# Performance work log

Measured on AMD Instinct MI355X. Metric: run time of the kernel, lower is better.

Reference implementation:

```python
import jax, jax.numpy as jnp
import numpy as np

B, N, C, H = 2, 2048, 1024, 16
D = C // H  # head_dim = 64
EPS = 1e-6


def _rope_freqs(n, d):
    inv_freq = 1.0 / (10000.0 ** (np.arange(0, d // 2, dtype=np.float32) * 2.0 / d))
    ang = np.arange(n, dtype=np.float32)[:, None] * inv_freq[None, :]  # [N, D/2]
    ang = np.concatenate([ang, ang], axis=-1)  # [N, D] (chunk-in-half convention)
    cos = jnp.asarray(np.cos(ang))[None, None]  # [1,1,N,D]
    sin = jnp.asarray(np.sin(ang))[None, None]
    return cos, sin


def setup_inputs() -> dict:
    key = jax.random.key(0)
    k1, k2, k3 = jax.random.split(key, 3)
    x = jax.random.normal(k1, (B, N, C), dtype=jnp.float32)
    w_qkv = jax.random.normal(k2, (3 * C, C), dtype=jnp.float32) * (C ** -0.5)
    w_proj = jax.random.normal(k3, (C, C), dtype=jnp.float32) * (C ** -0.5)
    b_proj = jnp.zeros((C,), dtype=jnp.float32)
    freqs_cos, freqs_sin = _rope_freqs(N, D)
    return {"x": x, "w_qkv": w_qkv, "w_proj": w_proj, "b_proj": b_proj,
            "freqs_cos": freqs_cos, "freqs_sin": freqs_sin}


def _layernorm(t):
    # affine-free LayerNorm over the last (head_dim) axis
    mu = jnp.mean(t, axis=-1, keepdims=True)
    var = jnp.var(t, axis=-1, keepdims=True)
    return (t - mu) * jax.lax.rsqrt(var + EPS)


def _rotate_half(t):
    t1, t2 = jnp.split(t, 2, axis=-1)
    return jnp.concatenate([-t2, t1], axis=-1)


def reference(x, w_qkv, w_proj, b_proj, freqs_cos, freqs_sin):
    b, n, c = x.shape
    qkv = jnp.einsum('bnc,kc->bnk', x, w_qkv)  # [B,N,3C]
    qkv = qkv.reshape(b, n, 3, H, D).transpose(2, 0, 3, 1, 4)  # [3,B,H,N,D]
    q, k, v = qkv[0], qkv[1], qkv[2]
    q = _layernorm(q)
    k = _layernorm(k)
    q = q * freqs_cos + _rotate_half(q) * freqs_sin
    k = k * freqs_cos + _rotate_half(k) * freqs_sin
    scale = D ** -0.5
    scores = jnp.einsum('bhqd,bhkd->bhqk', q, k) * scale  # [B,H,N,N]
    attn = jax.nn.softmax(scores, axis=-1)
    out = jnp.einsum('bhqk,bhkd->bhqd', attn, v)  # [B,H,N,D]
    out = out.transpose(0, 2, 1, 3).reshape(b, n, c)
    return jnp.einsum('bnc,oc->bno', out, w_proj) + b_proj
```

## Files before the change

kernel.cpp:

```cpp
#include <hip/hip_runtime.h>
#include <hip/hip_bf16.h>


typedef __bf16 bf16x8 __attribute__((ext_vector_type(8)));
typedef float f32x4 __attribute__((ext_vector_type(4)));
typedef float f32x16 __attribute__((ext_vector_type(16)));
typedef unsigned short us8 __attribute__((ext_vector_type(8)));
typedef unsigned short us4 __attribute__((ext_vector_type(4)));

static __device__ __forceinline__ unsigned short f2b(float f) {
  __hip_bfloat16 h = __float2bfloat16(f);
  return __builtin_bit_cast(unsigned short, h);
}
static __device__ __forceinline__ float b2f(unsigned short u) {
  __hip_bfloat16 h = __builtin_bit_cast(__hip_bfloat16, u);
  return __bfloat162float(h);
}

#if __has_builtin(__builtin_amdgcn_exp2f)
static __device__ __forceinline__ float fast_exp2(float x) { return __builtin_amdgcn_exp2f(x); }
#else
static __device__ __forceinline__ float fast_exp2(float x) { return exp2f(x); }
#endif

static __device__ __forceinline__ void async_copy16(void* lds, const void* g) {
  __builtin_amdgcn_global_load_lds(
      (const __attribute__((address_space(1))) void*)g,
      (__attribute__((address_space(3))) void*)lds, 16, 0, 0);
}

static __device__ __forceinline__ unsigned cvt_pk_bf16(float lo, float hi) {
  unsigned r;
  asm("v_cvt_pk_bf16_f32 %0, %1, %2" : "=v"(r) : "v"(lo), "v"(hi));
  return r;
}
static __device__ __forceinline__ void swap32(unsigned& x, unsigned& y) {
  asm("v_permlane32_swap_b32 %0, %1" : "+v"(x), "+v"(y));
}
static __device__ __forceinline__ float max3f(float a, float b, float c) {
  float d;
  asm("v_max3_f32 %0, %1, %2, %3" : "=v"(d) : "v"(a), "v"(b), "v"(c));
  return d;
}
static __device__ __forceinline__ float vmax16(const f32x16& v) {
  float a = max3f(v[0], v[1], v[2]);
  float b = max3f(v[3], v[4], v[5]);
  float c = max3f(v[6], v[7], v[8]);
  float d = max3f(v[9], v[10], v[11]);
  float e = max3f(v[12], v[13], v[14]);
  float x = max3f(a, b, c);
  float y = max3f(d, e, v[15]);
  return fmaxf(x, y);
}

__global__ __launch_bounds__(256) void cvt_bf16(
    const float* __restrict__ in, unsigned short* __restrict__ out, int n8) {
  int i = blockIdx.x * 256 + threadIdx.x;
  if (i >= n8) return;
  const float4* p = reinterpret_cast<const float4*>(in) + (size_t)i * 2;
  float4 a = p[0], b = p[1];
  us8 v;
  v[0] = f2b(a.x); v[1] = f2b(a.y); v[2] = f2b(a.z); v[3] = f2b(a.w);
  v[4] = f2b(b.x); v[5] = f2b(b.y); v[6] = f2b(b.z); v[7] = f2b(b.w);
  reinterpret_cast<us8*>(out)[i] = v;
}

template <int MODE>
__global__ __launch_bounds__(256, 2) void gemm_bt(
    const unsigned short* __restrict__ A, const unsigned short* __restrict__ Bw,
    const float* __restrict__ bias, void* __restrict__ Cout,
    int M, int Nn, int K) {
  __shared__ unsigned short a_sh[128 * 64];
  __shared__ unsigned short b_sh[128 * 64];
  const int tid = threadIdx.x;
  const int lane = tid & 63;
  const int w = tid >> 6;
  const int wr = w >> 1, wc = w & 1;
  const int l15 = lane & 15, l4 = lane >> 4;
  const int m0 = blockIdx.y * 128;
  const int n0 = blockIdx.x * 128;
  const int r8 = lane >> 3, c8 = lane & 7;

  f32x4 acc[4][4] = {};

  for (int k0 = 0; k0 < K; k0 += 64) {
#pragma unroll
    for (int p = 0; p < 8; ++p) {
      int s = p * 4 + w;
      if (s < 16) {
        int row = s * 8 + r8;
        async_copy16(&a_sh[s * 512],
                     &A[(size_t)(m0 + row) * K + k0 + ((c8 ^ (row & 7)) << 3)]);
      } else {
        int s2 = s - 16;
        int row = s2 * 8 + r8;
        async_copy16(&b_sh[s2 * 512],
                     &Bw[(size_t)(n0 + row) * K + k0 + ((c8 ^ (row & 7)) << 3)]);
      }
    }
    __syncthreads();
#pragma unroll
    for (int kk = 0; kk < 2; ++kk) {
      bf16x8 af[4], bfr[4];
#pragma unroll
      for (int mf = 0; mf < 4; ++mf) {
        int r = wr * 64 + mf * 16 + l15;
        af[mf] = *reinterpret_cast<const bf16x8*>(
            &a_sh[r * 64 + (((kk * 4 + l4) ^ (r & 7)) << 3)]);
      }
#pragma unroll
      for (int nf = 0; nf < 4; ++nf) {
        int r = wc * 64 + nf * 16 + l15;
        bfr[nf] = *reinterpret_cast<const bf16x8*>(
            &b_sh[r * 64 + (((kk * 4 + l4) ^ (r & 7)) << 3)]);
      }
#pragma unroll
      for (int mf = 0; mf < 4; ++mf)
#pragma unroll
        for (int nf = 0; nf < 4; ++nf)
          acc[mf][nf] = __builtin_amdgcn_mfma_f32_16x16x32_bf16(af[mf], bfr[nf], acc[mf][nf], 0, 0, 0);
    }
    __syncthreads();
  }
#pragma unroll
  for (int mf = 0; mf < 4; ++mf)
#pragma unroll
    for (int nf = 0; nf < 4; ++nf) {
      int col = n0 + wc * 64 + nf * 16 + l15;
#pragma unroll
      for (int j = 0; j < 4; ++j) {
        int row = m0 + wr * 64 + mf * 16 + l4 * 4 + j;
        float v = acc[mf][nf][j];
        if (MODE == 1) {
          v += bias[col];
          reinterpret_cast<float*>(Cout)[(size_t)row * Nn + col] = v;
        } else {
          reinterpret_cast<unsigned short*>(Cout)[(size_t)row * Nn + col] = f2b(v);
        }
      }
    }
}

__global__ __launch_bounds__(256) void ln_rope(
    const unsigned short* __restrict__ qkv,
    const float* __restrict__ fcos, const float* __restrict__ fsin,
    unsigned short* __restrict__ qo, unsigned short* __restrict__ ko)
{
  const int rid = blockIdx.x * 16 + (threadIdx.x >> 4);
  const int q16 = threadIdx.x & 15;
  const int h = rid & 15;
  const int three = (rid >> 4) & 1;
  const int n = (rid >> 5) & 2047;
  const int b = rid >> 16;
  const int m = b * 2048 + n;
  const int d0 = q16 * 4;
  us4 raw = *reinterpret_cast<const us4*>(
      &qkv[(size_t)m * 3072 + three * 1024 + h * 64 + d0]);
  float v[4];
#pragma unroll
  for (int e = 0; e < 4; ++e) v[e] = b2f(raw[e]);
  float s = v[0] + v[1] + v[2] + v[3];
  float s2 = v[0] * v[0] + v[1] * v[1] + v[2] * v[2] + v[3] * v[3];
#pragma unroll
  for (int off = 8; off; off >>= 1) {
    s += __shfl_xor(s, off);
    s2 += __shfl_xor(s2, off);
  }
  float mu = s * (1.f / 64.f);
  float var = s2 * (1.f / 64.f) - mu * mu;
  float inv = rsqrtf(var + 1e-6f);
  float t[4], other[4];
#pragma unroll
  for (int e = 0; e < 4; ++e) t[e] = (v[e] - mu) * inv;
#pragma unroll
  for (int e = 0; e < 4; ++e) other[e] = __shfl_xor(t[e], 8);
  float4 c4 = *reinterpret_cast<const float4*>(&fcos[n * 64 + d0]);
  float4 s4 = *reinterpret_cast<const float4*>(&fsin[n * 64 + d0]);
  float sgn = (d0 < 32) ? -1.f : 1.f;
  float sc = three ? 1.f : 0.18033688011112042f;
  us4 outv;
  outv[0] = f2b(sc * (t[0] * c4.x + sgn * other[0] * s4.x));
  outv[1] = f2b(sc * (t[1] * c4.y + sgn * other[1] * s4.y));
  outv[2] = f2b(sc * (t[2] * c4.z + sgn * other[2] * s4.z));
  outv[3] = f2b(sc * (t[3] * c4.w + sgn * other[3] * s4.w));
  unsigned short* dst = three ? ko : qo;
  *reinterpret_cast<us4*>(&dst[((size_t)(b * 16 + h) * 2048 + n) * 64 + d0]) = outv;
}

__global__ __launch_bounds__(256) void v_transpose(
    const unsigned short* __restrict__ qkv, unsigned short* __restrict__ vt) {
  __shared__ unsigned short sh[64][72];
  const int tid = threadIdx.x;
  const int bid = blockIdx.x;
  const int nt = bid & 31;
  const int h = (bid >> 5) & 15;
  const int b = bid >> 9;
#pragma unroll
  for (int p = 0; p < 2; ++p) {
    int g = p * 256 + tid;
    int i = g >> 3, c = g & 7;
    us8 v = *reinterpret_cast<const us8*>(
        &qkv[(size_t)(b * 2048 + nt * 64 + i) * 3072 + 2048 + h * 64 + c * 8]);
    *reinterpret_cast<us8*>(&sh[i][c * 8]) = v;
  }
  __syncthreads();
  const int bh = b * 16 + h;
#pragma unroll
  for (int p = 0; p < 2; ++p) {
    int g = p * 256 + tid;
    int d = g >> 3, c2 = g & 7;
    us8 v;
#pragma unroll
    for (int j = 0; j < 8; ++j) v[j] = sh[c2 * 8 + j][d];
    *reinterpret_cast<us8*>(&vt[((size_t)bh * 64 + d) * 2048 + nt * 64 + c2 * 8]) = v;
  }
}

__global__ __launch_bounds__(256, 2) void attn_kern(
    const unsigned short* __restrict__ Q,
    const unsigned short* __restrict__ Kk,
    const unsigned short* __restrict__ Vt,
    unsigned short* __restrict__ O)
{
  __shared__ unsigned short k_sh[2][128 * 64];
  __shared__ unsigned short v_sh[2][64 * 128];
  const int tid = threadIdx.x;
  const int lane = tid & 63;
  const int w = tid >> 6;
  const int l31 = lane & 31;
  const int H = lane >> 5;
  const int bid = blockIdx.x;
  const int wid = (bid & 7) * 64 + (bid >> 3);
  const int qt = wid & 15;
  const int bh = wid >> 4;
  const int h = bh & 15, b = bh >> 4;
  const unsigned short* qb = Q + (size_t)bh * 2048 * 64;
  const unsigned short* kb = Kk + (size_t)bh * 2048 * 64;
  const unsigned short* vb = Vt + (size_t)bh * 64 * 2048;
  const int tok = qt * 128 + w * 32 + l31;

  bf16x8 qf[4];
#pragma unroll
  for (int c = 0; c < 4; ++c)
    qf[c] = *reinterpret_cast<const bf16x8*>(&qb[(size_t)tok * 64 + c * 16 + H * 8]);

  f32x16 oT[2] = {};
  float mr = -1e30f, lr = 0.f;

  const int r8 = lane >> 3, cc8 = lane & 7;
  const int r4 = lane >> 4, cc16 = lane & 15;
#define ATTN_STAGE(KT, BUF)                                                           \
  {                                                                                   \
    _Pragma("unroll") for (int p = 0; p < 8; ++p) {                                   \
      int sseg = p * 4 + w;                                                           \
      if (sseg < 16) {                                                                \
        int row = sseg * 8 + r8;                                                      \
        async_copy16(&k_sh[BUF][sseg * 512],                                          \
                     &kb[(size_t)((KT) * 128 + row) * 64 + ((cc8 ^ (row & 7)) << 3)]);   \
      } else {                                                                        \
        int s2 = sseg - 16;                                                           \
        int row = s2 * 4 + r4;                                                        \
        async_copy16(&v_sh[BUF][s2 * 512],                                            \
                     &vb[(size_t)row * 2048 + (KT) * 128 + ((cc16 ^ (row & 7)) << 3)]);  \
      }                                                                               \
    }                                                                                 \
  }

  ATTN_STAGE(0, 0);
  __syncthreads();

  for (int kt = 0; kt < 16; ++kt) {
    const int cur = kt & 1;
    if (kt < 15) ATTN_STAGE(kt + 1, cur ^ 1);

    f32x16 sT[4] = {};
#pragma unroll
    for (int c = 0; c < 4; ++c) {
      int ch0 = 2 * c + H;
#pragma unroll
      for (int t = 0; t < 4; ++t) {
        int r = t * 32 + l31;
        bf16x8 ka = *reinterpret_cast<const bf16x8*>(
            &k_sh[cur][r * 64 + (((ch0) ^ (r & 7)) << 3)]);
        sT[t] = __builtin_amdgcn_mfma_f32_32x32x16_bf16(ka, qf[c], sT[t], 0, 0, 0);
      }
    }
    float tmax = fmaxf(fmaxf(vmax16(sT[0]), vmax16(sT[1])),
                       fmaxf(vmax16(sT[2]), vmax16(sT[3])));
    tmax = fmaxf(tmax, __shfl_xor(tmax, 32));
    if (__any(tmax > mr + 8.f)) {
      float mn = fmaxf(mr, tmax);
      float corr = fast_exp2(mr - mn);
      mr = mn;
      lr *= corr;
#pragma unroll
      for (int r = 0; r < 16; ++r) { oT[0][r] *= corr; oT[1][r] *= corr; }
    }
    float tsum = 0.f;
#pragma unroll
    for (int t = 0; t < 4; ++t)
#pragma unroll
      for (int r = 0; r < 16; ++r) {
        float p = fast_exp2(sT[t][r] - mr);
        sT[t][r] = p;
        tsum += p;
      }
    tsum += __shfl_xor(tsum, 32);
    lr += tsum;

    bf16x8 pB[8];
#pragma unroll
    for (int t = 0; t < 4; ++t)
#pragma unroll
      for (int half = 0; half < 2; ++half) {
        const int base = 8 * half;
        unsigned x0 = cvt_pk_bf16(sT[t][base + 0], sT[t][base + 1]);
        unsigned x1 = cvt_pk_bf16(sT[t][base + 2], sT[t][base + 3]);
        unsigned y0 = cvt_pk_bf16(sT[t][base + 4], sT[t][base + 5]);
        unsigned y1 = cvt_pk_bf16(sT[t][base + 6], sT[t][base + 7]);
        swap32(x0, y0);
        swap32(x1, y1);
        int4 packed = {(int)x0, (int)x1, (int)y0, (int)y1};
        pB[2 * t + half] = __builtin_bit_cast(bf16x8, packed);
      }
#pragma unroll
    for (int dt = 0; dt < 2; ++dt) {
      int r = dt * 32 + l31;
#pragma unroll
      for (int mi = 0; mi < 8; ++mi) {
        int ch = (mi * 2 + H) ^ (r & 7);
        bf16x8 va = *reinterpret_cast<const bf16x8*>(&v_sh[cur][r * 128 + (ch << 3)]);
        oT[dt] = __builtin_amdgcn_mfma_f32_32x32x16_bf16(va, pB[mi], oT[dt], 0, 0, 0);
      }
    }
    __syncthreads();
  }
  float invl = 1.f / lr;
#pragma unroll
  for (int dt = 0; dt < 2; ++dt)
#pragma unroll
    for (int rb = 0; rb < 4; ++rb) {
      us4 ov;
#pragma unroll
      for (int j = 0; j < 4; ++j) ov[j] = f2b(oT[dt][rb * 4 + j] * invl);
      *reinterpret_cast<us4*>(
          &O[((size_t)b * 2048 + tok) * 1024 + h * 64 + 32 * dt + 8 * rb + 4 * H]) = ov;
    }
#undef ATTN_STAGE
}

extern "C" void kernel_launch(void* const* d_in, const int* in_sizes, int n_in,
                              void* d_out, int out_size, void* d_ws, size_t ws_size,
                              hipStream_t stream) {
  (void)in_sizes; (void)n_in; (void)out_size; (void)ws_size;
  const float* x      = (const float*)d_in[0];
  const float* w_qkv  = (const float*)d_in[1];
  const float* w_proj = (const float*)d_in[2];
  const float* b_proj = (const float*)d_in[3];
  const float* fcos   = (const float*)d_in[4];
  const float* fsin   = (const float*)d_in[5];
  float* out = (float*)d_out;
  char* ws = (char*)d_ws;

  unsigned short* x_bf     = (unsigned short*)(ws + 0);
  unsigned short* wqkv_bf  = (unsigned short*)(ws + 8388608);
  unsigned short* wproj_bf = (unsigned short*)(ws + 14680064);
  unsigned short* qkv_bf   = (unsigned short*)(ws + 16777216);
  unsigned short* q_bf     = (unsigned short*)(ws + 41943040);
  unsigned short* k_bf     = (unsigned short*)(ws + 50331648);
  unsigned short* vt_bf    = (unsigned short*)(ws + 58720256);
  unsigned short* ao_bf    = (unsigned short*)(ws + 67108864);

  cvt_bf16<<<2048, 256, 0, stream>>>(x, x_bf, 4096 * 1024 / 8);
  cvt_bf16<<<1536, 256, 0, stream>>>(w_qkv, wqkv_bf, 3072 * 1024 / 8);
  cvt_bf16<<<512, 256, 0, stream>>>(w_proj, wproj_bf, 1024 * 1024 / 8);
  gemm_bt<0><<<dim3(24, 32), 256, 0, stream>>>(x_bf, wqkv_bf, nullptr, qkv_bf, 4096, 3072, 1024);
  ln_rope<<<8192, 256, 0, stream>>>(qkv_bf, fcos, fsin, q_bf, k_bf);
  v_transpose<<<1024, 256, 0, stream>>>(qkv_bf, vt_bf);
  attn_kern<<<512, 256, 0, stream>>>(q_bf, k_bf, vt_bf, ao_bf);
  gemm_bt<1><<<dim3(8, 32), 256, 0, stream>>>(ao_bf, wproj_bf, b_proj, out, 4096, 1024, 1024);
}
```

Baseline: 131.0 us.

## Fuse LayerNorm, RoPE and V transpose into QKV GEMM epilogue; add MFMA priority hints

The QKV GEMM epilogue now applies per-head LayerNorm, RoPE and the Q scale directly on the fp32 accumulators. It writes Q and K head-major and V transposed through swizzled shared memory. This removes the separate ln_rope and v_transpose kernels and the bf16 round-trip of the full QKV tensor through global memory. The attention kernel also raises wave priority around its MFMA blocks. The trade-off is a heavier epilogue with per-element cos/sin global loads, and LayerNorm statistics now computed before bf16 rounding, which changes numerics slightly.

```diff
diff --git a/kernel.cpp b/kernel.cpp
--- a/kernel.cpp
+++ b/kernel.cpp
@@ -65,10 +65,142 @@
   reinterpret_cast<us8*>(out)[i] = v;
 }
 
-template <int MODE>
-__global__ __launch_bounds__(256, 2) void gemm_bt(
+__global__ __launch_bounds__(256, 2) void gemm_qkv(
+    const unsigned short* __restrict__ A,
+    const unsigned short* __restrict__ Bw,
+    const float* __restrict__ fcos, const float* __restrict__ fsin,
+    unsigned short* __restrict__ qo, unsigned short* __restrict__ ko,
+    unsigned short* __restrict__ vt)
+{
+  __shared__ unsigned short a_sh[128 * 64];
+  __shared__ unsigned short b_sh[128 * 64];
+  const int tid = threadIdx.x;
+  const int lane = tid & 63;
+  const int w = tid >> 6;
+  const int wr = w >> 1, wc = w & 1;
+  const int l15 = lane & 15, l4 = lane >> 4;
+  const int m0 = blockIdx.y * 128;
+  const int n0 = blockIdx.x * 128;
+  const int r8 = lane >> 3, c8 = lane & 7;
+  const int K = 1024;
+
+  f32x4 acc[4][4] = {};
+
+  for (int k0 = 0; k0 < K; k0 += 64) {
+#pragma unroll
+    for (int p = 0; p < 8; ++p) {
+      int s = p * 4 + w;
+      if (s < 16) {
+        int row = s * 8 + r8;
+        async_copy16(&a_sh[s * 512],
+                     &A[(size_t)(m0 + row) * K + k0 + ((c8 ^ (row & 7)) << 3)]);
+      } else {
+        int s2 = s - 16;
+        int row = s2 * 8 + r8;
+        async_copy16(&b_sh[s2 * 512],
+                     &Bw[(size_t)(n0 + row) * K + k0 + ((c8 ^ (row & 7)) << 3)]);
+      }
+    }
+    __syncthreads();
+#pragma unroll
+    for (int kk = 0; kk < 2; ++kk) {
+      bf16x8 af[4], bfr[4];
+#pragma unroll
+      for (int mf = 0; mf < 4; ++mf) {
+        int r = wr * 64 + mf * 16 + l15;
+        af[mf] = *reinterpret_cast<const bf16x8*>(
+            &a_sh[r * 64 + (((kk * 4 + l4) ^ (r & 7)) << 3)]);
+      }
+#pragma unroll
+      for (int nf = 0; nf < 4; ++nf) {
+        int r = wc * 64 + nf * 16 + l15;
+        bfr[nf] = *reinterpret_cast<const bf16x8*>(
+            &b_sh[r * 64 + (((kk * 4 + l4) ^ (r & 7)) << 3)]);
+      }
+#pragma unroll
+      for (int mf = 0; mf < 4; ++mf)
+#pragma unroll
+        for (int nf = 0; nf < 4; ++nf)
+          acc[mf][nf] = __builtin_amdgcn_mfma_f32_16x16x32_bf16(af[mf], bfr[nf], acc[mf][nf], 0, 0, 0);
+    }
+    __syncthreads();
+  }
+
+  const int colbase = n0 + wc * 64;
+  const int three = colbase >> 10;
+  const int hh = (colbase >> 6) & 15;
+  const int b_ = m0 >> 11;
+  const int nbase = (m0 & 2047) + wr * 64;
+  unsigned short* ep = ((w < 2) ? a_sh : b_sh) + (w & 1) * 4096;
+  const int cch = lane & 7, rb2 = lane >> 3;
+
+  if (three < 2) {
+    const float sc = three ? 1.f : 0.18033688011112042f;
+#pragma unroll
+    for (int mf = 0; mf < 4; ++mf) {
+#pragma unroll
+      for (int j = 0; j < 4; ++j) {
+        float a0 = acc[mf][0][j], a1 = acc[mf][1][j];
+        float a2 = acc[mf][2][j], a3 = acc[mf][3][j];
+        float s1 = (a0 + a1) + (a2 + a3);
+        float s2 = (a0 * a0 + a1 * a1) + (a2 * a2 + a3 * a3);
+#pragma unroll
+        for (int off = 8; off; off >>= 1) {
+          s1 += __shfl_xor(s1, off);
+          s2 += __shfl_xor(s2, off);
+        }
+        float mu = s1 * (1.f / 64.f);
+        float inv = rsqrtf(s2 * (1.f / 64.f) - mu * mu + 1e-6f);
+        int rloc = mf * 16 + l4 * 4 + j;
+        int n = nbase + rloc;
+        const float* cp = &fcos[(size_t)n * 64];
+        const float* sp = &fsin[(size_t)n * 64];
+#pragma unroll
+        for (int nf = 0; nf < 4; ++nf) {
+          int d = nf * 16 + l15;
+          float t = (acc[mf][nf][j] - mu) * inv;
+          float tp = (acc[mf][nf ^ 2][j] - mu) * inv;
+          float r = sc * (t * cp[d] + ((nf < 2) ? -tp : tp) * sp[d]);
+          ep[rloc * 64 + ((((d >> 3) ^ (rloc & 7)) << 3) | (d & 7))] = f2b(r);
+        }
+      }
+    }
+    unsigned short* dst =
+        (three ? ko : qo) + (size_t)(b_ * 16 + hh) * 2048 * 64;
+#pragma unroll
+    for (int i = 0; i < 8; ++i) {
+      int row = i * 8 + rb2;
+      us8 vd = *reinterpret_cast<const us8*>(
+          &ep[row * 64 + ((cch ^ (row & 7)) << 3)]);
+      *reinterpret_cast<us8*>(&dst[(size_t)(nbase + row) * 64 + cch * 8]) = vd;
+    }
+  } else {
+#pragma unroll
+    for (int mf = 0; mf < 4; ++mf)
+#pragma unroll
+      for (int nf = 0; nf < 4; ++nf) {
+        int d = nf * 16 + l15;
+#pragma unroll
+        for (int j = 0; j < 4; ++j) {
+          int nl = mf * 16 + l4 * 4 + j;
+          ep[d * 64 + ((((nl >> 3) ^ (d & 7)) << 3) | (nl & 7))] =
+              f2b(acc[mf][nf][j]);
+        }
+      }
+    unsigned short* dst = vt + (size_t)(b_ * 16 + hh) * 64 * 2048;
+#pragma unroll
+    for (int i = 0; i < 8; ++i) {
+      int d = i * 8 + rb2;
+      us8 vd = *reinterpret_cast<const us8*>(
+          &ep[d * 64 + ((cch ^ (d & 7)) << 3)]);
+      *reinterpret_cast<us8*>(&dst[(size_t)d * 2048 + nbase + cch * 8]) = vd;
+    }
+  }
+}
+
+__global__ __launch_bounds__(256, 2) void gemm_proj(
     const unsigned short* __restrict__ A, const unsigned short* __restrict__ Bw,
-    const float* __restrict__ bias, void* __restrict__ Cout,
+    const float* __restrict__ bias, float* __restrict__ Cout,
     int M, int Nn, int K) {
   __shared__ unsigned short a_sh[128 * 64];
   __shared__ unsigned short b_sh[128 * 64];
@@ -130,90 +262,9 @@
 #pragma unroll
       for (int j = 0; j < 4; ++j) {
         int row = m0 + wr * 64 + mf * 16 + l4 * 4 + j;
-        float v = acc[mf][nf][j];
-        if (MODE == 1) {
-          v += bias[col];
-          reinterpret_cast<float*>(Cout)[(size_t)row * Nn + col] = v;
-        } else {
-          reinterpret_cast<unsigned short*>(Cout)[(size_t)row * Nn + col] = f2b(v);
-        }
-      }
-    }
-}
-
-__global__ __launch_bounds__(256) void ln_rope(
-    const unsigned short* __restrict__ qkv,
-    const float* __restrict__ fcos, const float* __restrict__ fsin,
-    unsigned short* __restrict__ qo, unsigned short* __restrict__ ko)
-{
-  const int rid = blockIdx.x * 16 + (threadIdx.x >> 4);
-  const int q16 = threadIdx.x & 15;
-  const int h = rid & 15;
-  const int three = (rid >> 4) & 1;
-  const int n = (rid >> 5) & 2047;
-  const int b = rid >> 16;
-  const int m = b * 2048 + n;
-  const int d0 = q16 * 4;
-  us4 raw = *reinterpret_cast<const us4*>(
-      &qkv[(size_t)m * 3072 + three * 1024 + h * 64 + d0]);
-  float v[4];
-#pragma unroll
-  for (int e = 0; e < 4; ++e) v[e] = b2f(raw[e]);
-  float s = v[0] + v[1] + v[2] + v[3];
-  float s2 = v[0] * v[0] + v[1] * v[1] + v[2] * v[2] + v[3] * v[3];
-#pragma unroll
-  for (int off = 8; off; off >>= 1) {
-    s += __shfl_xor(s, off);
-    s2 += __shfl_xor(s2, off);
-  }
-  float mu = s * (1.f / 64.f);
-  float var = s2 * (1.f / 64.f) - mu * mu;
-  float inv = rsqrtf(var + 1e-6f);
-  float t[4], other[4];
-#pragma unroll
-  for (int e = 0; e < 4; ++e) t[e] = (v[e] - mu) * inv;
-#pragma unroll
-  for (int e = 0; e < 4; ++e) other[e] = __shfl_xor(t[e], 8);
-  float4 c4 = *reinterpret_cast<const float4*>(&fcos[n * 64 + d0]);
-  float4 s4 = *reinterpret_cast<const float4*>(&fsin[n * 64 + d0]);
-  float sgn = (d0 < 32) ? -1.f : 1.f;
-  float sc = three ? 1.f : 0.18033688011112042f;
-  us4 outv;
-  outv[0] = f2b(sc * (t[0] * c4.x + sgn * other[0] * s4.x));
-  outv[1] = f2b(sc * (t[1] * c4.y + sgn * other[1] * s4.y));
-  outv[2] = f2b(sc * (t[2] * c4.z + sgn * other[2] * s4.z));
-  outv[3] = f2b(sc * (t[3] * c4.w + sgn * other[3] * s4.w));
-  unsigned short* dst = three ? ko : qo;
-  *reinterpret_cast<us4*>(&dst[((size_t)(b * 16 + h) * 2048 + n) * 64 + d0]) = outv;
-}
-
-__global__ __launch_bounds__(256) void v_transpose(
-    const unsigned short* __restrict__ qkv, unsigned short* __restrict__ vt) {
-  __shared__ unsigned short sh[64][72];
-  const int tid = threadIdx.x;
-  const int bid = blockIdx.x;
-  const int nt = bid & 31;
-  const int h = (bid >> 5) & 15;
-  const int b = bid >> 9;
-#pragma unroll
-  for (int p = 0; p < 2; ++p) {
-    int g = p * 256 + tid;
-    int i = g >> 3, c = g & 7;
-    us8 v = *reinterpret_cast<const us8*>(
-        &qkv[(size_t)(b * 2048 + nt * 64 + i) * 3072 + 2048 + h * 64 + c * 8]);
-    *reinterpret_cast<us8*>(&sh[i][c * 8]) = v;
-  }
-  __syncthreads();
-  const int bh = b * 16 + h;
-#pragma unroll
-  for (int p = 0; p < 2; ++p) {
-    int g = p * 256 + tid;
-    int d = g >> 3, c2 = g & 7;
-    us8 v;
-#pragma unroll
-    for (int j = 0; j < 8; ++j) v[j] = sh[c2 * 8 + j][d];
-    *reinterpret_cast<us8*>(&vt[((size_t)bh * 64 + d) * 2048 + nt * 64 + c2 * 8]) = v;
-  }
+        Cout[(size_t)row * Nn + col] = acc[mf][nf][j] + bias[col];
+      }
+    }
 }
 
 __global__ __launch_bounds__(256, 2) void attn_kern(
@@ -274,6 +325,7 @@
     if (kt < 15) ATTN_STAGE(kt + 1, cur ^ 1);
 
     f32x16 sT[4] = {};
+    __builtin_amdgcn_s_setprio(1);
 #pragma unroll
     for (int c = 0; c < 4; ++c) {
       int ch0 = 2 * c + H;
@@ -285,6 +337,7 @@
         sT[t] = __builtin_amdgcn_mfma_f32_32x32x16_bf16(ka, qf[c], sT[t], 0, 0, 0);
       }
     }
+    __builtin_amdgcn_s_setprio(0);
     float tmax = fmaxf(fmaxf(vmax16(sT[0]), vmax16(sT[1])),
                        fmaxf(vmax16(sT[2]), vmax16(sT[3])));
     tmax = fmaxf(tmax, __shfl_xor(tmax, 32));
@@ -323,6 +376,7 @@
         int4 packed = {(int)x0, (int)x1, (int)y0, (int)y1};
         pB[2 * t + half] = __builtin_bit_cast(bf16x8, packed);
       }
+    __builtin_amdgcn_s_setprio(1);
 #pragma unroll
     for (int dt = 0; dt < 2; ++dt) {
       int r = dt * 32 + l31;
@@ -333,6 +387,7 @@
         oT[dt] = __builtin_amdgcn_mfma_f32_32x32x16_bf16(va, pB[mi], oT[dt], 0, 0, 0);
       }
     }
+    __builtin_amdgcn_s_setprio(0);
     __syncthreads();
   }
   float invl = 1.f / lr;
@@ -365,18 +420,17 @@
   unsigned short* x_bf     = (unsigned short*)(ws + 0);
   unsigned short* wqkv_bf  = (unsigned short*)(ws + 8388608);
   unsigned short* wproj_bf = (unsigned short*)(ws + 14680064);
-  unsigned short* qkv_bf   = (unsigned short*)(ws + 16777216);
-  unsigned short* q_bf     = (unsigned short*)(ws + 41943040);
-  unsigned short* k_bf     = (unsigned short*)(ws + 50331648);
-  unsigned short* vt_bf    = (unsigned short*)(ws + 58720256);
-  unsigned short* ao_bf    = (unsigned short*)(ws + 67108864);
+  unsigned short* q_bf     = (unsigned short*)(ws + 16777216);
+  unsigned short* k_bf     = (unsigned short*)(ws + 25165824);
+  unsigned short* vt_bf    = (unsigned short*)(ws + 33554432);
+  unsigned short* ao_bf    = (unsigned short*)(ws + 41943040);
 
   cvt_bf16<<<2048, 256, 0, stream>>>(x, x_bf, 4096 * 1024 / 8);
   cvt_bf16<<<1536, 256, 0, stream>>>(w_qkv, wqkv_bf, 3072 * 1024 / 8);
   cvt_bf16<<<512, 256, 0, stream>>>(w_proj, wproj_bf, 1024 * 1024 / 8);
-  gemm_bt<0><<<dim3(24, 32), 256, 0, stream>>>(x_bf, wqkv_bf, nullptr, qkv_bf, 4096, 3072, 1024);
-  ln_rope<<<8192, 256, 0, stream>>>(qkv_bf, fcos, fsin, q_bf, k_bf);
-  v_transpose<<<1024, 256, 0, stream>>>(qkv_bf, vt_bf);
+  gemm_qkv<<<dim3(24, 32), 256, 0, stream>>>(x_bf, wqkv_bf, fcos, fsin,
+                                             q_bf, k_bf, vt_bf);
   attn_kern<<<512, 256, 0, stream>>>(q_bf, k_bf, vt_bf, ao_bf);
-  gemm_bt<1><<<dim3(8, 32), 256, 0, stream>>>(ao_bf, wproj_bf, b_proj, out, 4096, 1024, 1024);
-}
+  gemm_proj<<<dim3(8, 32), 256, 0, stream>>>(ao_bf, wproj_bf, b_proj, out,
+                                             4096, 1024, 1024);
+}
```

Result: faster. 124.4 us (-5.1%).
